# Kernel optimization log

Measured on AMD Instinct MI355X. Metric: run time of the kernel, lower is better.

The kernel has to match this reference:

```python
import jax, jax.numpy as jnp
import numpy as np

N, D, K = 262144, 64, 64
TEMPERATURE = 1.0
PRIOR_P = 0.1
PRIOR_LOGVAR0 = -2.0  # prior_logvar_0 buffer (constant per-dim)
LOG2PI = float(np.log(2.0 * np.pi))


def setup_inputs() -> dict:
    key = jax.random.key(0)
    k1, k2, k3, k4 = jax.random.split(key, 4)
    prior_phi_probs = jnp.full((D,), PRIOR_P, dtype=jnp.float32)
    phi_logits = jnp.log(prior_phi_probs / (1.0 - prior_phi_probs))  # init = prior log-odds
    return {
        "X": jax.random.normal(k1, (N, D), dtype=jnp.float32),
        "u_noise": jax.random.uniform(k2, (D,), dtype=jnp.float32),
        "phi_logits": phi_logits,
        "q_mu": jax.random.normal(k3, (K, D), dtype=jnp.float32),
        "q_logvar": jnp.full((K, D), -1.0, dtype=jnp.float32),
        "pi_logits": jnp.ones((K,), dtype=jnp.float32),
        "prior_phi_probs": prior_phi_probs,
    }


def reference(X, u_noise, phi_logits, q_mu, q_logvar, pi_logits, prior_phi_probs):
    n = X.shape[0]
    # Gumbel-sigmoid sample of phi (per-dimension gate), shape (D,)
    gumbel = -jnp.log(-jnp.log(u_noise + 1e-9) + 1e-9)
    phi = jax.nn.sigmoid((phi_logits + gumbel) / TEMPERATURE)

    logvar = jnp.clip(q_logvar, -5.0, 5.0)            # (K, D)
    inv_var = jnp.exp(-logvar)                        # (K, D)

    # sum_d phi_d * log N(x_d | mu_kd, var_kd), decomposed to GEMM form so the
    # full (N, K, D) tensor is never materialized:
    #   -0.5 * [ sum_d phi*(LOG2PI + logvar_kd)  +  sum_d phi*(x-mu)^2/var_kd ]
    a = phi[None, :] * inv_var                        # (K, D)
    quad = (jnp.einsum('nd,kd->nk', X * X, a)
            - 2.0 * jnp.einsum('nd,kd->nk', X, q_mu * a)
            + jnp.sum(q_mu * q_mu * a, axis=1)[None, :])          # (N, K)
    const_k = jnp.sum(phi[None, :] * (LOG2PI + logvar), axis=1)   # (K,)
    lp_cluster = -0.5 * (const_k[None, :] + quad)                 # (N, K)

    # background term: sum_d (1-phi_d) * log N(x_d | 0, exp(prior_logvar_0)); per-sample scalar
    inv_var0 = float(np.exp(-PRIOR_LOGVAR0))
    lp_bg = -0.5 * jnp.sum((1.0 - phi)[None, :]
                           * (LOG2PI + PRIOR_LOGVAR0 + X * X * inv_var0), axis=1)  # (N,)

    log_p_x_given_z = lp_cluster + lp_bg[:, None]     # (N, K)

    pi = jax.nn.softmax(pi_logits)
    log_joint = log_p_x_given_z + jnp.log(pi + 1e-9)[None, :]
    log_likelihood = jnp.sum(jax.nn.logsumexp(log_joint, axis=1))

    q_phi = jnp.clip(jax.nn.sigmoid(phi_logits), 1e-6, 1.0 - 1e-6)
    p_phi = jnp.clip(prior_phi_probs, 1e-6, 1.0 - 1e-6)
    kl_phi = jnp.sum(q_phi * (jnp.log(q_phi) - jnp.log(p_phi))
                     + (1.0 - q_phi) * (jnp.log(1.0 - q_phi) - jnp.log(1.0 - p_phi))) * n

    loss = -log_likelihood + kl_phi
    return (loss, q_phi, log_p_x_given_z)
```

## Files before the change

### kernel.cpp

```cpp
#include <hip/hip_runtime.h>
#include <hip/hip_bf16.h>
#include <math.h>

#define N_SAMPLES 262144
#define DDIM 64
#define KDIM 64
#define NBLOCKS 4096

#define LOG2PI 1.8378770664093453f
#define PRIOR_LV0 -2.0f
#define IV0 7.389056098930650f


#define WS_C     4096
#define WS_LPI   4160
#define WS_PART  4224
#define WS_STAGE 4224

typedef __attribute__((ext_vector_type(8))) short short8;
typedef __attribute__((ext_vector_type(4))) float floatx4;

static __device__ inline unsigned short f2bf_bits(float f) {
  union { float f; unsigned u; } v; v.f = f;
  unsigned r = v.u + 0x7fffu + ((v.u >> 16) & 1u);
  return (unsigned short)(r >> 16);
}

__global__ __launch_bounds__(256) void setup_frags(
    const float* __restrict__ u_noise, const float* __restrict__ phi_logits,
    const float* __restrict__ q_mu, const float* __restrict__ q_logvar,
    const float* __restrict__ pi_logits, float* __restrict__ ws) {
  __shared__ float sPhi[DDIM];
  __shared__ float sR[DDIM];
  __shared__ float sBeta;
  __shared__ float sPart[4][KDIM];
  int tid = threadIdx.x;

  if (tid < 64) {
    int d = tid;
    float u = u_noise[d];
    float g = -__logf(-__logf(u + 1e-9f) + 1e-9f);
    float phi = 1.0f / (1.0f + __expf(-(phi_logits[d] + g)));
    sPhi[d] = phi;
    sR[d] = -0.5f * (1.0f - phi) * IV0;

    float betap = -0.5f * (1.0f - phi) * (LOG2PI + PRIOR_LV0);
    #pragma unroll
    for (int o = 1; o < 64; o <<= 1) betap += __shfl_xor(betap, o, 64);
    if (d == 0) sBeta = betap;

    float l = pi_logits[d];
    float m = l;
    #pragma unroll
    for (int o = 1; o < 64; o <<= 1) m = fmaxf(m, __shfl_xor(m, o, 64));
    float e = __expf(l - m);
    float s = e;
    #pragma unroll
    for (int o = 1; o < 64; o <<= 1) s += __shfl_xor(s, o, 64);
    ws[WS_LPI + d] = __logf(e / s + 1e-9f);
  }
  __syncthreads();

  int k = tid & 63, seg = tid >> 6;
  float ap = 0.0f;
  for (int dd = 0; dd < 16; ++dd) {
    int d = seg * 16 + dd;
    float lv = fminf(fmaxf(q_logvar[k * DDIM + d], -5.0f), 5.0f);
    float iv = __expf(-lv);
    float a = sPhi[d] * iv;
    float mu = q_mu[k * DDIM + d];
    ws[WS_STAGE + d * 128 + k]      = -0.5f * a + sR[d];
    ws[WS_STAGE + d * 128 + 64 + k] = mu * a;
    ap += sPhi[d] * (LOG2PI + lv) + mu * mu * a;
  }
  sPart[seg][k] = ap;
  __syncthreads();
  if (tid < 64) {
    float alpha = sPart[0][tid] + sPart[1][tid] + sPart[2][tid] + sPart[3][tid];
    ws[WS_C + tid] = -0.5f * alpha + sBeta;
  }

  unsigned short* bsw = (unsigned short*)ws;
  #pragma unroll
  for (int p = 0; p < 4; ++p) {
    int pr = p * 256 + tid;
    int s  = pr >> 6;
    int l  = pr & 63;
    int kc = s >> 2, tl = s & 3;
    int q  = l >> 4, nn = l & 15;
    int col = tl * 16 + nn;
    int bk  = kc * 32 + q * 8;
    #pragma unroll
    for (int j = 0; j < 8; ++j) {
      int r = bk + j;
      float val = (r < 64) ? ws[WS_STAGE + r * 128 + col]
                           : ws[WS_STAGE + (r - 64) * 128 + 64 + col];
      bsw[pr * 8 + j] = f2bf_bits(val);
    }
  }
}

__global__ __launch_bounds__(256, 4) void gmm_main(
    const float* __restrict__ X, const float* __restrict__ ws,
    float* __restrict__ out) {
  __shared__ float sRed[4];
  int tid  = threadIdx.x;
  int lane = tid & 63;
  int w    = tid >> 6;
  int n    = lane & 15;
  int q    = lane >> 4;
  long rbase = ((long)blockIdx.x * 4 + w) * 16;

  const float* xr = X + (rbase + n) * DDIM;
  float4 xa0 = *(const float4*)(xr + q * 8);
  float4 xa1 = *(const float4*)(xr + q * 8 + 4);
  float4 xb0 = *(const float4*)(xr + 32 + q * 8);
  float4 xb1 = *(const float4*)(xr + 32 + q * 8 + 4);

  short8 a[4];
  {
    float xa[8] = {xa0.x, xa0.y, xa0.z, xa0.w, xa1.x, xa1.y, xa1.z, xa1.w};
    float xb[8] = {xb0.x, xb0.y, xb0.z, xb0.w, xb1.x, xb1.y, xb1.z, xb1.w};
    #pragma unroll
    for (int j = 0; j < 8; ++j) {
      a[0][j] = (short)f2bf_bits(xa[j] * xa[j]);
      a[1][j] = (short)f2bf_bits(xb[j] * xb[j]);
      a[2][j] = (short)f2bf_bits(xa[j]);
      a[3][j] = (short)f2bf_bits(xb[j]);
    }
  }

  const short8* Bf = (const short8*)ws;
  floatx4 acc[4];
  #pragma unroll
  for (int t = 0; t < 4; ++t) acc[t] = (floatx4){0.f, 0.f, 0.f, 0.f};
  #pragma unroll
  for (int kc = 0; kc < 4; ++kc) {
    #pragma unroll
    for (int t = 0; t < 4; ++t) {
      short8 b = Bf[(kc * 4 + t) * 64 + lane];
      acc[t] = __builtin_amdgcn_mfma_f32_16x16x32_bf16(a[kc], b, acc[t], 0, 0, 0);
    }
  }

  float cb[4], lpi[4];
  #pragma unroll
  for (int t = 0; t < 4; ++t) {
    cb[t]  = ws[WS_C + t * 16 + n];
    lpi[t] = ws[WS_LPI + t * 16 + n];
  }
  float* lp = out + 1 + DDIM;
  float rowacc = 0.0f;
  #pragma unroll
  for (int reg = 0; reg < 4; ++reg) {
    long row = rbase + q * 4 + reg;
    float o0 = acc[0][reg] + cb[0];
    float o1 = acc[1][reg] + cb[1];
    float o2 = acc[2][reg] + cb[2];
    float o3 = acc[3][reg] + cb[3];
    long off = row * KDIM + n;
    lp[off]      = o0;
    lp[off + 16] = o1;
    lp[off + 32] = o2;
    lp[off + 48] = o3;
    float v0 = o0 + lpi[0], v1 = o1 + lpi[1], v2 = o2 + lpi[2], v3 = o3 + lpi[3];
    float m = fmaxf(fmaxf(v0, v1), fmaxf(v2, v3));
    #pragma unroll
    for (int o = 1; o <= 8; o <<= 1) m = fmaxf(m, __shfl_xor(m, o, 64));
    float s = __expf(v0 - m) + __expf(v1 - m) + __expf(v2 - m) + __expf(v3 - m);
    #pragma unroll
    for (int o = 1; o <= 8; o <<= 1) s += __shfl_xor(s, o, 64);
    if (n == 0) rowacc += m + __logf(s);
  }
  float t2 = (n == 0) ? rowacc : 0.0f;
  t2 += __shfl_xor(t2, 16, 64);
  t2 += __shfl_xor(t2, 32, 64);
  if (lane == 0) sRed[w] = t2;
  __syncthreads();
  if (tid == 0) {
    float* wsp = (float*)ws;
    wsp[WS_PART + blockIdx.x] = sRed[0] + sRed[1] + sRed[2] + sRed[3];
  }
}

__global__ __launch_bounds__(256) void finalize_kernel(
    const float* __restrict__ phi_logits, const float* __restrict__ prior_p,
    const float* __restrict__ ws, float* __restrict__ out) {
  __shared__ float sW[4];
  __shared__ float sKl;
  int tid = threadIdx.x;
  int lane = tid & 63, w = tid >> 6;

  float s = 0.0f;
  #pragma unroll
  for (int i = 0; i < NBLOCKS / 256; ++i)
    s += ws[WS_PART + i * 256 + tid];
  #pragma unroll
  for (int o = 1; o < 64; o <<= 1) s += __shfl_xor(s, o, 64);
  if (lane == 0) sW[w] = s;

  if (tid < 64) {
    int d = tid;
    float qp = 1.0f / (1.0f + __expf(-phi_logits[d]));
    qp = fminf(fmaxf(qp, 1e-6f), 1.0f - 1e-6f);
    out[1 + d] = qp;
    float pp = fminf(fmaxf(prior_p[d], 1e-6f), 1.0f - 1e-6f);
    float klp = qp * (__logf(qp) - __logf(pp)) +
                (1.0f - qp) * (__logf(1.0f - qp) - __logf(1.0f - pp));
    #pragma unroll
    for (int o = 1; o < 64; o <<= 1) klp += __shfl_xor(klp, o, 64);
    if (d == 0) sKl = klp * (float)N_SAMPLES;
  }
  __syncthreads();
  if (tid == 0) out[0] = sKl - (sW[0] + sW[1] + sW[2] + sW[3]);
}

extern "C" void kernel_launch(void* const* d_in, const int* in_sizes, int n_in,
                              void* d_out, int out_size, void* d_ws, size_t ws_size,
                              hipStream_t stream) {
  const float* X           = (const float*)d_in[0];
  const float* u_noise     = (const float*)d_in[1];
  const float* phi_logits  = (const float*)d_in[2];
  const float* q_mu        = (const float*)d_in[3];
  const float* q_logvar    = (const float*)d_in[4];
  const float* pi_logits   = (const float*)d_in[5];
  const float* prior_p     = (const float*)d_in[6];
  float* out = (float*)d_out;
  float* ws  = (float*)d_ws;

  setup_frags<<<1, 256, 0, stream>>>(u_noise, phi_logits, q_mu, q_logvar,
                                     pi_logits, ws);
  gmm_main<<<NBLOCKS, 256, 0, stream>>>(X, ws, out);
  finalize_kernel<<<1, 256, 0, stream>>>(phi_logits, prior_p, ws, out);
}
```

Measured before the change: 141.5 us.

## Process two row tiles per wave and build B fragments directly in setup

Each wave now handles 32 rows (two 16-row MFMA tiles), loading all of X up front and reusing the B fragments and bias registers, with half as many blocks. The block-level shared-memory reduction and barrier are dropped in favour of per-wave partial sums, and finalize sums four times as many partials. The setup kernel builds the bf16 B fragments straight from q_mu and q_logvar with vector loads instead of going through a float staging area. The aim is more in-flight loads per wave and less launch and barrier overhead, at the cost of higher register pressure and fewer waves overall.

```diff
diff --git a/kernel.cpp b/kernel.cpp
--- a/kernel.cpp
+++ b/kernel.cpp
@@ -5,7 +5,8 @@
 #define N_SAMPLES 262144
 #define DDIM 64
 #define KDIM 64
-#define NBLOCKS 4096
+#define NBLOCKS 2048
+#define NPART (NBLOCKS * 4)
 
 #define LOG2PI 1.8378770664093453f
 #define PRIOR_LV0 -2.0f
@@ -15,7 +16,6 @@
 #define WS_C     4096
 #define WS_LPI   4160
 #define WS_PART  4224
-#define WS_STAGE 4224
 
 typedef __attribute__((ext_vector_type(8))) short short8;
 typedef __attribute__((ext_vector_type(4))) float floatx4;
@@ -61,87 +61,85 @@
   }
   __syncthreads();
 
-  int k = tid & 63, seg = tid >> 6;
-  float ap = 0.0f;
-  for (int dd = 0; dd < 16; ++dd) {
-    int d = seg * 16 + dd;
-    float lv = fminf(fmaxf(q_logvar[k * DDIM + d], -5.0f), 5.0f);
-    float iv = __expf(-lv);
-    float a = sPhi[d] * iv;
-    float mu = q_mu[k * DDIM + d];
-    ws[WS_STAGE + d * 128 + k]      = -0.5f * a + sR[d];
-    ws[WS_STAGE + d * 128 + 64 + k] = mu * a;
-    ap += sPhi[d] * (LOG2PI + lv) + mu * mu * a;
-  }
-  sPart[seg][k] = ap;
+  {
+    int k = tid & 63, seg = tid >> 6;
+    const float* lvp = q_logvar + k * DDIM + seg * 16;
+    const float* mup = q_mu + k * DDIM + seg * 16;
+    float ap = 0.0f;
+    #pragma unroll
+    for (int dd = 0; dd < 16; ++dd) {
+      int d = seg * 16 + dd;
+      float lv = fminf(fmaxf(lvp[dd], -5.0f), 5.0f);
+      float mu = mup[dd];
+      ap += sPhi[d] * (LOG2PI + lv) + mu * mu * sPhi[d] * __expf(-lv);
+    }
+    sPart[seg][k] = ap;
+  }
+
+  unsigned short* bsw = (unsigned short*)ws;
+  #pragma unroll
+  for (int p = 0; p < 4; ++p) {
+    int pr = p * 256 + tid;
+    int s = pr >> 6, l = pr & 63;
+    int kc = s >> 2, tl = s & 3, q = l >> 4, nn = l & 15;
+    int k = tl * 16 + nn;
+    int dbase = (kc & 1) * 32 + q * 8;
+    const float* lvp = q_logvar + k * DDIM + dbase;
+    float4 lv0 = *(const float4*)lvp;
+    float4 lv1 = *(const float4*)(lvp + 4);
+    float lvv[8] = {lv0.x, lv0.y, lv0.z, lv0.w, lv1.x, lv1.y, lv1.z, lv1.w};
+    short r8[8];
+    if (kc < 2) {
+      #pragma unroll
+      for (int j = 0; j < 8; ++j) {
+        int d = dbase + j;
+        float lv = fminf(fmaxf(lvv[j], -5.0f), 5.0f);
+        r8[j] = (short)f2bf_bits(-0.5f * sPhi[d] * __expf(-lv) + sR[d]);
+      }
+    } else {
+      const float* mup = q_mu + k * DDIM + dbase;
+      float4 mu0 = *(const float4*)mup;
+      float4 mu1 = *(const float4*)(mup + 4);
+      float muv[8] = {mu0.x, mu0.y, mu0.z, mu0.w, mu1.x, mu1.y, mu1.z, mu1.w};
+      #pragma unroll
+      for (int j = 0; j < 8; ++j) {
+        int d = dbase + j;
+        float lv = fminf(fmaxf(lvv[j], -5.0f), 5.0f);
+        r8[j] = (short)f2bf_bits(muv[j] * sPhi[d] * __expf(-lv));
+      }
+    }
+    ((short8*)bsw)[pr] = (short8){r8[0], r8[1], r8[2], r8[3],
+                                  r8[4], r8[5], r8[6], r8[7]};
+  }
+
   __syncthreads();
   if (tid < 64) {
     float alpha = sPart[0][tid] + sPart[1][tid] + sPart[2][tid] + sPart[3][tid];
     ws[WS_C + tid] = -0.5f * alpha + sBeta;
   }
-
-  unsigned short* bsw = (unsigned short*)ws;
-  #pragma unroll
-  for (int p = 0; p < 4; ++p) {
-    int pr = p * 256 + tid;
-    int s  = pr >> 6;
-    int l  = pr & 63;
-    int kc = s >> 2, tl = s & 3;
-    int q  = l >> 4, nn = l & 15;
-    int col = tl * 16 + nn;
-    int bk  = kc * 32 + q * 8;
-    #pragma unroll
-    for (int j = 0; j < 8; ++j) {
-      int r = bk + j;
-      float val = (r < 64) ? ws[WS_STAGE + r * 128 + col]
-                           : ws[WS_STAGE + (r - 64) * 128 + 64 + col];
-      bsw[pr * 8 + j] = f2bf_bits(val);
-    }
-  }
 }
 
 __global__ __launch_bounds__(256, 4) void gmm_main(
     const float* __restrict__ X, const float* __restrict__ ws,
     float* __restrict__ out) {
-  __shared__ float sRed[4];
   int tid  = threadIdx.x;
   int lane = tid & 63;
   int w    = tid >> 6;
   int n    = lane & 15;
   int q    = lane >> 4;
-  long rbase = ((long)blockIdx.x * 4 + w) * 16;
-
-  const float* xr = X + (rbase + n) * DDIM;
-  float4 xa0 = *(const float4*)(xr + q * 8);
-  float4 xa1 = *(const float4*)(xr + q * 8 + 4);
-  float4 xb0 = *(const float4*)(xr + 32 + q * 8);
-  float4 xb1 = *(const float4*)(xr + 32 + q * 8 + 4);
-
-  short8 a[4];
-  {
-    float xa[8] = {xa0.x, xa0.y, xa0.z, xa0.w, xa1.x, xa1.y, xa1.z, xa1.w};
-    float xb[8] = {xb0.x, xb0.y, xb0.z, xb0.w, xb1.x, xb1.y, xb1.z, xb1.w};
-    #pragma unroll
-    for (int j = 0; j < 8; ++j) {
-      a[0][j] = (short)f2bf_bits(xa[j] * xa[j]);
-      a[1][j] = (short)f2bf_bits(xb[j] * xb[j]);
-      a[2][j] = (short)f2bf_bits(xa[j]);
-      a[3][j] = (short)f2bf_bits(xb[j]);
-    }
-  }
-
-  const short8* Bf = (const short8*)ws;
-  floatx4 acc[4];
-  #pragma unroll
-  for (int t = 0; t < 4; ++t) acc[t] = (floatx4){0.f, 0.f, 0.f, 0.f};
-  #pragma unroll
-  for (int kc = 0; kc < 4; ++kc) {
-    #pragma unroll
-    for (int t = 0; t < 4; ++t) {
-      short8 b = Bf[(kc * 4 + t) * 64 + lane];
-      acc[t] = __builtin_amdgcn_mfma_f32_16x16x32_bf16(a[kc], b, acc[t], 0, 0, 0);
-    }
-  }
+  long wbase = ((long)blockIdx.x * 4 + w) * 32;
+
+  const float* xr0 = X + (wbase + n) * DDIM;
+  const float* xr1 = xr0 + 16 * DDIM;
+  float4 raw[2][4];
+  raw[0][0] = *(const float4*)(xr0 + q * 8);
+  raw[0][1] = *(const float4*)(xr0 + q * 8 + 4);
+  raw[0][2] = *(const float4*)(xr0 + 32 + q * 8);
+  raw[0][3] = *(const float4*)(xr0 + 32 + q * 8 + 4);
+  raw[1][0] = *(const float4*)(xr1 + q * 8);
+  raw[1][1] = *(const float4*)(xr1 + q * 8 + 4);
+  raw[1][2] = *(const float4*)(xr1 + 32 + q * 8);
+  raw[1][3] = *(const float4*)(xr1 + 32 + q * 8 + 4);
 
   float cb[4], lpi[4];
   #pragma unroll
@@ -149,37 +147,68 @@
     cb[t]  = ws[WS_C + t * 16 + n];
     lpi[t] = ws[WS_LPI + t * 16 + n];
   }
+
+  const short8* Bf = (const short8*)ws;
   float* lp = out + 1 + DDIM;
   float rowacc = 0.0f;
-  #pragma unroll
-  for (int reg = 0; reg < 4; ++reg) {
-    long row = rbase + q * 4 + reg;
-    float o0 = acc[0][reg] + cb[0];
-    float o1 = acc[1][reg] + cb[1];
-    float o2 = acc[2][reg] + cb[2];
-    float o3 = acc[3][reg] + cb[3];
-    long off = row * KDIM + n;
-    lp[off]      = o0;
-    lp[off + 16] = o1;
-    lp[off + 32] = o2;
-    lp[off + 48] = o3;
-    float v0 = o0 + lpi[0], v1 = o1 + lpi[1], v2 = o2 + lpi[2], v3 = o3 + lpi[3];
-    float m = fmaxf(fmaxf(v0, v1), fmaxf(v2, v3));
-    #pragma unroll
-    for (int o = 1; o <= 8; o <<= 1) m = fmaxf(m, __shfl_xor(m, o, 64));
-    float s = __expf(v0 - m) + __expf(v1 - m) + __expf(v2 - m) + __expf(v3 - m);
-    #pragma unroll
-    for (int o = 1; o <= 8; o <<= 1) s += __shfl_xor(s, o, 64);
-    if (n == 0) rowacc += m + __logf(s);
-  }
+
+  #pragma unroll
+  for (int tt = 0; tt < 2; ++tt) {
+    long rbase = wbase + tt * 16;
+    short8 a[4];
+    {
+      float xa[8] = {raw[tt][0].x, raw[tt][0].y, raw[tt][0].z, raw[tt][0].w,
+                     raw[tt][1].x, raw[tt][1].y, raw[tt][1].z, raw[tt][1].w};
+      float xb[8] = {raw[tt][2].x, raw[tt][2].y, raw[tt][2].z, raw[tt][2].w,
+                     raw[tt][3].x, raw[tt][3].y, raw[tt][3].z, raw[tt][3].w};
+      #pragma unroll
+      for (int j = 0; j < 8; ++j) {
+        a[0][j] = (short)f2bf_bits(xa[j] * xa[j]);
+        a[1][j] = (short)f2bf_bits(xb[j] * xb[j]);
+        a[2][j] = (short)f2bf_bits(xa[j]);
+        a[3][j] = (short)f2bf_bits(xb[j]);
+      }
+    }
+    floatx4 acc[4];
+    #pragma unroll
+    for (int t = 0; t < 4; ++t) acc[t] = (floatx4){0.f, 0.f, 0.f, 0.f};
+    #pragma unroll
+    for (int kc = 0; kc < 4; ++kc) {
+      #pragma unroll
+      for (int t = 0; t < 4; ++t) {
+        short8 b = Bf[(kc * 4 + t) * 64 + lane];
+        acc[t] = __builtin_amdgcn_mfma_f32_16x16x32_bf16(a[kc], b, acc[t], 0, 0, 0);
+      }
+    }
+    #pragma unroll
+    for (int reg = 0; reg < 4; ++reg) {
+      long row = rbase + q * 4 + reg;
+      float o0 = acc[0][reg] + cb[0];
+      float o1 = acc[1][reg] + cb[1];
+      float o2 = acc[2][reg] + cb[2];
+      float o3 = acc[3][reg] + cb[3];
+      long off = row * KDIM + n;
+      lp[off]      = o0;
+      lp[off + 16] = o1;
+      lp[off + 32] = o2;
+      lp[off + 48] = o3;
+      float v0 = o0 + lpi[0], v1 = o1 + lpi[1], v2 = o2 + lpi[2], v3 = o3 + lpi[3];
+      float m = fmaxf(fmaxf(v0, v1), fmaxf(v2, v3));
+      #pragma unroll
+      for (int o = 1; o <= 8; o <<= 1) m = fmaxf(m, __shfl_xor(m, o, 64));
+      float s = __expf(v0 - m) + __expf(v1 - m) + __expf(v2 - m) + __expf(v3 - m);
+      #pragma unroll
+      for (int o = 1; o <= 8; o <<= 1) s += __shfl_xor(s, o, 64);
+      if (n == 0) rowacc += m + __logf(s);
+    }
+  }
+
   float t2 = (n == 0) ? rowacc : 0.0f;
   t2 += __shfl_xor(t2, 16, 64);
   t2 += __shfl_xor(t2, 32, 64);
-  if (lane == 0) sRed[w] = t2;
-  __syncthreads();
-  if (tid == 0) {
+  if (lane == 0) {
     float* wsp = (float*)ws;
-    wsp[WS_PART + blockIdx.x] = sRed[0] + sRed[1] + sRed[2] + sRed[3];
+    wsp[WS_PART + blockIdx.x * 4 + w] = t2;
   }
 }
 
@@ -193,7 +222,7 @@
 
   float s = 0.0f;
   #pragma unroll
-  for (int i = 0; i < NBLOCKS / 256; ++i)
+  for (int i = 0; i < NPART / 256; ++i)
     s += ws[WS_PART + i * 256 + tid];
   #pragma unroll
   for (int o = 1; o < 64; o <<= 1) s += __shfl_xor(s, o, 64);
```

Result: no change. 144.0 us (+1.7%).
